# Optimization experiments

Measured on AMD Instinct MI355X. Metric: run time of the kernel, lower is better.

Reference implementation:

```python
import jax, jax.numpy as jnp
import numpy as np

V, E, H = 32000, 256, 512   # vocab, embed_dim, hidden_dim
B, S, T = 16, 512, 128      # batch, src_len, tgt_len
PAD = 0
H2 = 2 * H                  # decoder hidden size


def setup_inputs() -> dict:
    key = jax.random.key(0)
    ks = jax.random.split(key, 20)
    g = lambda k, shape: jax.random.normal(k, shape, dtype=jnp.float32) * 0.05
    emb = g(ks[0], (V, E)).at[PAD].set(0.0)  # padding_idx row zeroed
    inp = {
        "src": jax.random.randint(ks[18], (B, S), 0, V, dtype=jnp.int32),
        "tgt": jax.random.randint(ks[19], (B, T), 0, V, dtype=jnp.int32),
        "emb": emb,
        # encoder forward direction (torch gate order i,f,g,o)
        "Wih_f": g(ks[1], (4 * H, E)), "Whh_f": g(ks[2], (4 * H, H)),
        "bih_f": g(ks[3], (4 * H,)),   "bhh_f": g(ks[4], (4 * H,)),
        # encoder backward direction
        "Wih_b": g(ks[5], (4 * H, E)), "Whh_b": g(ks[6], (4 * H, H)),
        "bih_b": g(ks[7], (4 * H,)),   "bhh_b": g(ks[8], (4 * H,)),
        # decoder LSTM: input E+2H, hidden 2H
        "Wih_d": g(ks[9], (4 * H2, E + H2)), "Whh_d": g(ks[10], (4 * H2, H2)),
        "bih_d": g(ks[11], (4 * H2,)),       "bhh_d": g(ks[12], (4 * H2,)),
        # attention Linear(4H -> 2H)
        "Wa": g(ks[13], (H2, 2 * H2)), "ba": g(ks[14], (H2,)),
        # output Linear(2H -> V)
        "Wo": g(ks[15], (V, H2)), "bo": g(ks[16], (V,)),
    }
    return inp


def _lstm_cell(x, h, c, Wih, Whh, bih, bhh):
    z = x @ Wih.T + h @ Whh.T + bih + bhh
    i, f, g, o = jnp.split(z, 4, axis=-1)
    c = jax.nn.sigmoid(f) * c + jax.nn.sigmoid(i) * jnp.tanh(g)
    h = jax.nn.sigmoid(o) * jnp.tanh(c)
    return h, c


def _lstm_scan(xs, h0, c0, Wih, Whh, bih, bhh):
    def step(carry, x):
        h, c = _lstm_cell(x, carry[0], carry[1], Wih, Whh, bih, bhh)
        return (h, c), h
    (hT, cT), hs = jax.lax.scan(step, (h0, c0), xs)
    return hs, hT, cT


def reference(src, tgt, emb, Wih_f, Whh_f, bih_f, bhh_f, Wih_b, Whh_b, bih_b, bhh_b,
              Wih_d, Whh_d, bih_d, bhh_d, Wa, ba, Wo, bo):
    z = jnp.zeros((B, H), dtype=emb.dtype)
    xs = emb[src].transpose(1, 0, 2)                       # [S,B,E]
    hs_f, hTf, _ = _lstm_scan(xs,        z, z, Wih_f, Whh_f, bih_f, bhh_f)
    hs_b, hTb, _ = _lstm_scan(xs[::-1],  z, z, Wih_b, Whh_b, bih_b, bhh_b)
    enc_out = jnp.concatenate([hs_f, hs_b[::-1]], -1).transpose(1, 0, 2)  # [B,S,2H]
    h = jnp.concatenate([hTf, hTb], -1)                    # decoder h0 [B,2H]
    c = jnp.zeros_like(h)  # note: original reuses encoder c_n; see combined c0 below
    # original uses c_n (last cells) as decoder c0:
    _, _, cTf = _lstm_scan(xs, z, z, Wih_f, Whh_f, bih_f, bhh_f)[1], None, None
    # recompute cleanly (scan already returned cT above; redo properly):
    hs_f2, hTf2, cTf2 = _lstm_scan(xs,       z, z, Wih_f, Whh_f, bih_f, bhh_f)
    hs_b2, hTb2, cTb2 = _lstm_scan(xs[::-1], z, z, Wih_b, Whh_b, bih_b, bhh_b)
    c = jnp.concatenate([cTf2, cTb2], -1)

    Wa_h, Wa_e = Wa[:, :H2], Wa[:, H2:]
    enc_proj = jnp.einsum('bsd,kd->bsk', enc_out, Wa_e) + ba  # [B,S,2H]

    dec_xs = emb[tgt[:, :T - 1]].transpose(1, 0, 2)        # [T-1,B,E] teacher-forced

    def dec_step(carry, x):
        h, c = carry
        energy = jnp.tanh(enc_proj + (h @ Wa_h.T)[:, None, :])  # [B,S,2H]
        w = jax.nn.softmax(energy.sum(-1), axis=1)              # [B,S]
        ctx = jnp.einsum('bs,bsd->bd', w, enc_out)              # [B,2H]
        xi = jnp.concatenate([x, ctx], -1)                      # [B,E+2H]
        h, c = _lstm_cell(xi, h, c, Wih_d, Whh_d, bih_d, bhh_d)
        pred = h @ Wo.T + bo                                    # [B,V]
        return (h, c), pred

    _, preds = jax.lax.scan(dec_step, (h, c), dec_xs)           # [T-1,B,V]
    outputs = jnp.concatenate(
        [jnp.zeros((B, 1, V), dtype=preds.dtype), preds.transpose(1, 0, 2)], axis=1)
    return outputs
```

## Files before the change

### kernel.cpp

```cpp
#include <hip/hip_runtime.h>

typedef unsigned int uint;
typedef unsigned short ushort;
typedef unsigned long long ull;
typedef __attribute__((ext_vector_type(8))) short bf16x8;
typedef __attribute__((ext_vector_type(4))) float f32x4;

static constexpr int V_ = 32000, E_ = 256, H_ = 512, B_ = 16, S_ = 512, T_ = 128;
static constexpr int H2_ = 1024, G4_ = 2048, D4_ = 4096, KXI_ = 2304;
static constexpr int DSTEPS = T_ - 1;
static constexpr int MD = 2048;
static constexpr int NWG_DEC = 256;
static constexpr float LOG2E = 1.4426950408889634f;
static constexpr int ASTR = 2312;

#define DEVFN __device__ __forceinline__

DEVFN ushort f2bf(float f){ uint u = __builtin_bit_cast(uint, f); u += 0x7fffu + ((u>>16)&1u); return (ushort)(u>>16); }
DEVFN float bf2f(ushort h){ uint u = ((uint)h)<<16; return __builtin_bit_cast(float, u); }
DEVFN float fsig(float x){ float e = __builtin_amdgcn_exp2f(-LOG2E*x); return __builtin_amdgcn_rcpf(1.f+e); }
DEVFN float ftanh(float x){ x = fminf(15.f,fmaxf(-15.f,x)); float e = __builtin_amdgcn_exp2f(2.f*LOG2E*x); return (e-1.f)*__builtin_amdgcn_rcpf(e+1.f); }
DEVFN f32x4 mfma16(bf16x8 a, bf16x8 b, f32x4 c){ return __builtin_amdgcn_mfma_f32_16x16x32_bf16(a,b,c,0,0,0); }

struct ull2v{ ull x, y; };
DEVFN ull ald64(const void* p){ return __hip_atomic_load((const ull*)p, __ATOMIC_RELAXED, __HIP_MEMORY_SCOPE_AGENT); }
DEVFN uint ald32u(const uint* p){ return __hip_atomic_load(p, __ATOMIC_RELAXED, __HIP_MEMORY_SCOPE_AGENT); }
DEVFN float ald_f32(const float* p){ uint v = __hip_atomic_load((const uint*)p, __ATOMIC_RELAXED, __HIP_MEMORY_SCOPE_AGENT); return __builtin_bit_cast(float, v); }
DEVFN bf16x8 ald_bf16x8(const ushort* p){ ull2v v{ald64(p), ald64(p+4)}; return __builtin_bit_cast(bf16x8, v); }
DEVFN void ast32(float* p, float v){ __hip_atomic_store(p, v, __ATOMIC_RELAXED, __HIP_MEMORY_SCOPE_AGENT); }
DEVFN void ast16(ushort* p, ushort v){ __hip_atomic_store(p, v, __ATOMIC_RELAXED, __HIP_MEMORY_SCOPE_AGENT); }
DEVFN void astu(uint* p, uint v){ __hip_atomic_store(p, v, __ATOMIC_RELAXED, __HIP_MEMORY_SCOPE_AGENT); }
DEVFN uint afadd(uint* p){ return __hip_atomic_fetch_add(p, 1u, __ATOMIC_RELAXED, __HIP_MEMORY_SCOPE_AGENT); }

DEVFN void dbar(uint* flags, int wgid, int tid, uint& rnd){
  __syncthreads();
  if (tid==0){
    uint* gcnt = flags + (wgid>>4)*16;
    uint* rcnt = flags + 256;
    uint* rgen = flags + 272;
    uint a = afadd(gcnt);
    if (a == rnd*16u+15u){
      uint r = afadd(rcnt);
      if (r == rnd*16u+15u) afadd(rgen);
    }
    while (ald32u(rgen) <= rnd) __builtin_amdgcn_s_sleep(1);
  }
  rnd++;
  __syncthreads();
}

__global__ void k_init(uint* __restrict__ flags, ushort* __restrict__ hgf, ushort* __restrict__ hgb){
  int i = blockIdx.x*256 + threadIdx.x;
  if (i < 512) flags[i] = 0;
  if (i < 2*B_*H_){ hgf[i]=0; hgb[i]=0; }
}

__global__ void k_embed(const int* __restrict__ src, const int* __restrict__ tgt,
                        const float* __restrict__ emb, ushort* __restrict__ Xb, ushort* __restrict__ DXb){
  int r = blockIdx.x, tid = threadIdx.x;
  if (r < S_*B_){
    int s = r>>4, b = r&15;
    int id = src[b*S_+s];
    Xb[(size_t)r*E_+tid] = f2bf(emb[(size_t)id*E_+tid]);
  } else {
    int r2 = r - S_*B_;
    int t = r2>>4, b = r2&15;
    int id = tgt[b*T_+t];
    DXb[(size_t)r2*E_+tid] = f2bf(emb[(size_t)id*E_+tid]);
  }
}

__global__ void k_cvt_encw(const float* __restrict__ src, ushort* __restrict__ dst){
  int d = blockIdx.x;
  int wg = d>>7, r = d&127;
  int w = r>>4, jj=(r>>2)&3, g=r&3;
  int srow = g*H_ + wg*32 + w*4 + jj;
  for (int c = threadIdx.x; c < E_; c += 256)
    dst[(size_t)d*E_ + c] = f2bf(src[(size_t)srow*E_ + c]);
}

__global__ void k_bias_encp(const float* __restrict__ bih, const float* __restrict__ bhh, float* __restrict__ dst){
  int d = blockIdx.x*256 + threadIdx.x;
  int wg = d>>7, r = d&127;
  int w = r>>4, jj=(r>>2)&3, g=r&3;
  int srow = g*H_ + wg*32 + w*4 + jj;
  dst[d] = bih[srow]+bhh[srow];
}

__global__ void k_cvt_decw(const float* __restrict__ Wih_d, const float* __restrict__ Whh_d,
                           ushort* __restrict__ dst){
  int d = blockIdx.x;
  int wg = d>>4, r = d&15, jj = r>>2, g = r&3;
  int srow = g*H2_ + wg*4 + jj;
  for (int c = threadIdx.x; c < KXI_; c += 256){
    float v = (c < E_+H2_) ? Wih_d[(size_t)srow*(E_+H2_) + c] : Whh_d[(size_t)srow*H2_ + (c - (E_+H2_))];
    dst[(size_t)d*KXI_ + c] = f2bf(v);
  }
}

__global__ void k_bias_decp(const float* __restrict__ bih, const float* __restrict__ bhh, float* __restrict__ dst){
  int d = blockIdx.x*256 + threadIdx.x;
  int wg = d>>4, r = d&15, jj = r>>2, g = r&3;
  int srow = g*H2_ + wg*4 + jj;
  dst[d] = bih[srow]+bhh[srow];
}

__global__ void k_cvt_strided(const float* __restrict__ src, ushort* __restrict__ dst,
                              int cols, int sld, int soff, int dld, int doff){
  int r = blockIdx.x;
  for (int c = threadIdx.x; c < cols; c += 256)
    dst[(size_t)r*dld + doff + c] = f2bf(src[(size_t)r*sld + soff + c]);
}

__global__ void k_zero_t0(float* __restrict__ out){
  int i = blockIdx.x*256 + threadIdx.x;
  if (i < B_*V_){ int b = i / V_, v = i - b*V_; out[(size_t)b*T_*V_ + v] = 0.f; }
}

template<int MODE>
__global__ __launch_bounds__(256) void gemm128(const ushort* __restrict__ A, const ushort* __restrict__ Bm,
    const float* __restrict__ bias, void* __restrict__ outp, int M, int N, int K, int Mvalid){
  __shared__ __align__(16) ushort As[128*32];
  __shared__ __align__(16) ushort Bs[128*32];
  int tid = threadIdx.x;
  int wave = tid>>6, lane = tid&63;
  int m0 = blockIdx.y*128, n0 = blockIdx.x*128;
  int wm = wave>>1, wn = wave&1;
  int col = lane&15, rg = lane>>4;
  f32x4 acc[4][4];
  #pragma unroll
  for (int i=0;i<4;i++)
    #pragma unroll
    for (int j=0;j<4;j++) acc[i][j] = {0.f,0.f,0.f,0.f};
  for (int k0=0;k0<K;k0+=32){
    __syncthreads();
    #pragma unroll
    for (int j=0;j<2;j++){
      int li = j*256+tid;
      int row = li>>2, ko = (li&3)*8;
      *(bf16x8*)(As + li*8) = *(const bf16x8*)(A + (size_t)(m0+row)*K + k0 + ko);
      *(bf16x8*)(Bs + li*8) = *(const bf16x8*)(Bm + (size_t)(n0+row)*K + k0 + ko);
    }
    __syncthreads();
    bf16x8 af[4], bfr[4];
    #pragma unroll
    for (int f=0;f<4;f++){
      af[f]  = *(const bf16x8*)(As + (wm*64+f*16+col)*32 + rg*8);
      bfr[f] = *(const bf16x8*)(Bs + (wn*64+f*16+col)*32 + rg*8);
    }
    #pragma unroll
    for (int fm=0;fm<4;fm++)
      #pragma unroll
      for (int fn=0;fn<4;fn++)
        acc[fm][fn] = mfma16(af[fm], bfr[fn], acc[fm][fn]);
  }
  #pragma unroll
  for (int fm=0;fm<4;fm++){
    int mrow = m0 + wm*64 + fm*16 + rg*4;
    #pragma unroll
    for (int fn=0;fn<4;fn++){
      int gcol = n0 + wn*64 + fn*16 + col;
      float bv = bias ? bias[gcol] : 0.f;
      #pragma unroll
      for (int i=0;i<4;i++){
        float v = acc[fm][fn][i] + bv;
        int grow = mrow + i;
        if (MODE==0) ((float*)outp)[(size_t)grow*N + gcol] = v;
        else if (MODE==1) ((ushort*)outp)[(size_t)grow*N + gcol] = f2bf(v);
        else if (MODE==3) ((ushort*)outp)[(size_t)(grow>>4)*(16*2048) + gcol*16 + (grow&15)] = f2bf(v);
        else { if (grow < Mvalid){ int b = grow&15, t = grow>>4;
               ((float*)outp)[(size_t)b*T_*V_ + (size_t)(t+1)*V_ + gcol] = v; } }
      }
    }
  }
}

__global__ __launch_bounds__(512) void k_enc_persist(
    const ushort* __restrict__ Xgf, const ushort* __restrict__ Xgb,
    const float* __restrict__ Whhf, const float* __restrict__ Whhb,
    ushort* __restrict__ enc, ushort* __restrict__ enct,
    ushort* __restrict__ hbuf1, float* __restrict__ cbuf0,
    ushort* __restrict__ hgf, ushort* __restrict__ hgb,
    uint* __restrict__ flags){
  const int dir = blockIdx.x >> 4;
  const int wg  = blockIdx.x & 15;
  const ushort* Xg = dir ? Xgb : Xgf;
  const float* Whh = dir ? Whhb : Whhf;
  ushort* hg = dir ? hgb : hgf;
  uint* cnt = flags + 384 + dir*32;
  uint* gen = cnt + 16;
  __shared__ __align__(16) ushort Wlds[128*512];
  __shared__ __align__(16) ushort hls[16*512];
  int tid = threadIdx.x;
  for (int it=0; it<32; ++it){
    int r = it*4 + (tid>>7), ct = tid&127;
    int w_ = r>>4, jj=(r>>2)&3, g=r&3;
    int srow = g*H_ + wg*32 + w_*4 + jj;
    float4 v = *(const float4*)(Whh + (size_t)srow*H_ + ct*4);
    ushort4 o; o.x=f2bf(v.x); o.y=f2bf(v.y); o.z=f2bf(v.z); o.w=f2bf(v.w);
    int byte = (r*1024 + ct*8) ^ ((r&7)<<4);
    *(ushort4*)((char*)Wlds + byte) = o;
  }
  int w = tid>>6, lane = tid&63, colL = lane&15, rg = lane>>4;
  int gg = colL&3;
  uint rnd = 0;
  float cst[4];
  #pragma unroll
  for (int i=0;i<4;i++) cst[i]=0.f;
  __syncthreads();
  for (int t=0;t<S_;++t){
    int pos = dir ? (S_-1-t) : t;
    const ushort* hsrc = hg + (t&1)*B_*H_;
    bf16x8 hv[2];
    #pragma unroll
    for (int k2=0;k2<2;k2++){
      int idx = tid + k2*512;
      hv[k2] = ald_bf16x8(hsrc + (idx>>6)*H_ + (idx&63)*8);
    }
    int colg = wg*128 + w*16 + colL;
    ushort4 xv = *(const ushort4*)(Xg + ((size_t)pos*2048 + colg)*16 + rg*4);
    f32x4 acc;
    acc[0]=bf2f(xv.x); acc[1]=bf2f(xv.y); acc[2]=bf2f(xv.z); acc[3]=bf2f(xv.w);
    #pragma unroll
    for (int k2=0;k2<2;k2++){
      int idx = tid + k2*512;
      int byte = ((idx>>6)*1024 + (idx&63)*16) ^ (((idx>>6)&7)<<4);
      *(bf16x8*)((char*)hls + byte) = hv[k2];
    }
    __syncthreads();
    int rowb = w*16 + colL;
    int base = rowb*1024 + rg*16, xm = (rowb&7)<<4;
    int hbase = colL*1024 + rg*16, hxm = (colL&7)<<4;
    #pragma unroll
    for (int kt=0;kt<16;kt++){
      bf16x8 afv = *(const bf16x8*)((const char*)hls + ((hbase + kt*64) ^ hxm));
      bf16x8 bfv = *(const bf16x8*)((const char*)Wlds + ((base + kt*64) ^ xm));
      acc = mfma16(afv, bfv, acc);
    }
    ushort* hdst = hg + ((t+1)&1)*B_*H_;
    #pragma unroll
    for (int i=0;i<4;i++){
      float v0 = acc[i];
      float v1 = __shfl_xor(v0, 1);
      float v2 = __shfl_xor(v0, 2);
      float v3 = __shfl_xor(v1, 2);
      float zi = gg==0?v0: gg==1?v1: gg==2?v2: v3;
      float zf = (gg^1)==0?v0: (gg^1)==1?v1: (gg^1)==2?v2: v3;
      float zg = (gg^2)==0?v0: (gg^2)==1?v1: (gg^2)==2?v2: v3;
      float zo = (gg^3)==0?v0: (gg^3)==1?v1: (gg^3)==2?v2: v3;
      float cc = fsig(zf)*cst[i] + fsig(zi)*ftanh(zg);
      cst[i] = cc;
      float h = fsig(zo)*ftanh(cc);
      if (gg==0){
        int j = wg*32 + w*4 + (colL>>2);
        int b = rg*4+i;
        ushort hb = f2bf(h);
        enc[((size_t)b*S_ + pos)*H2_ + dir*H_ + j] = hb;
        enct[((size_t)b*H2_ + dir*H_ + j)*S_ + pos] = hb;
        ast16(&hdst[b*H_ + j], hb);
        if (t==S_-1){
          hbuf1[b*H2_ + dir*H_ + j] = hb;
          cbuf0[b*H2_ + dir*H_ + j] = cc;
        }
      }
    }
    if (t != S_-1){
      __syncthreads();
      if (tid==0){
        asm volatile("s_waitcnt vmcnt(0)" ::: "memory");
        uint a = afadd(cnt);
        if (a == rnd*16u+15u) afadd(gen);
        while (ald32u(gen) <= rnd) __builtin_amdgcn_s_sleep(1);
      }
      rnd++;
      __syncthreads();
    }
  }
}

__global__ __launch_bounds__(512) void k_dec(
    const float* __restrict__ P, const ushort* __restrict__ WaH,
    const ushort* __restrict__ Wd, const float* __restrict__ bsd,
    const ushort* __restrict__ enct, const ushort* __restrict__ DXb,
    const float* __restrict__ cbuf0, ushort* __restrict__ hbuf,
    ushort* __restrict__ ctxbuf, float* __restrict__ qbuf,
    float* __restrict__ scores, ushort* __restrict__ hsd,
    uint* __restrict__ flags){
  __shared__ __align__(16) ushort AB[16*ASTR];
  __shared__ __align__(16) float pr[8*256];
  __shared__ float redz[256];
  __shared__ float qls[1024];
  __shared__ float wls[512];
  __shared__ float part[512];
  __shared__ float red[16];
  __shared__ float cst[64];
  int wgid = blockIdx.x, tid = threadIdx.x;
  int w = tid>>6, lane = tid&63, colL = lane&15, rg = lane>>4;
  uint rnd = 0;
  if (tid < 64){
    int jj = tid>>4, b = tid&15;
    cst[tid] = cbuf0[b*H2_ + wgid*4 + jj];
  }
  for (int st=0; st<DSTEPS; ++st){
    ushort* hprev = hbuf + ((st+1)&1)*B_*H2_;
    if (wgid >= 64 && wgid < 128){
      int n0 = (wgid-64)*16;
      bf16x8 af[4];
      #pragma unroll
      for (int kt=0;kt<4;kt++)
        af[kt] = ald_bf16x8(hprev + colL*H2_ + w*128 + kt*32 + rg*8);
      f32x4 acc = {0.f,0.f,0.f,0.f};
      const ushort* Bp = WaH + (size_t)(n0+colL)*H2_ + w*128 + rg*8;
      #pragma unroll
      for (int kt=0;kt<4;kt++)
        acc = mfma16(af[kt], *(const bf16x8*)(Bp + kt*32), acc);
      *(f32x4*)&pr[w*256 + lane*4] = acc;
      __syncthreads();
      if (tid < 256){
        float s = pr[tid];
        #pragma unroll
        for (int w8=1;w8<8;w8++) s += pr[w8*256 + tid];
        int l = tid>>2, i = tid&3;
        ast32(&qbuf[(size_t)((l>>4)*4 + i)*H2_ + n0 + (l&15)], s);
      }
    }
    dbar(flags, wgid, tid, rnd);
    {
      int b = wgid>>4, wc = wgid&15;
      ull q2 = ald64((const ull*)(qbuf + (size_t)b*H2_) + tid);
      *(ull*)&qls[tid*2] = q2;
      __syncthreads();
      f32x4 qv[4];
      #pragma unroll
      for (int u=0;u<4;u++) qv[u] = *(const f32x4*)&qls[lane*16 + u*4];
      int rbase = b*S_ + wc*32 + w*4;
      #pragma unroll
      for (int rr=0;rr<4;rr++){
        int r = rbase + rr;
        const float4* Pr = (const float4*)(P + (size_t)r*H2_) + lane*4;
        float s = 0.f;
        #pragma unroll
        for (int u=0;u<4;u++){
          float4 pv = Pr[u];
          s += ftanh(pv.x+qv[u][0])+ftanh(pv.y+qv[u][1])+ftanh(pv.z+qv[u][2])+ftanh(pv.w+qv[u][3]);
        }
        #pragma unroll
        for (int o=32;o;o>>=1) s += __shfl_xor(s,o);
        if (lane==0) ast32(&scores[r], s);
      }
    }
    dbar(flags, wgid, tid, rnd);
    {
      int b = wgid>>4, cc = wgid&15;
      float sc = ald_f32(scores + b*S_ + tid);
      float m = sc;
      #pragma unroll
      for (int o=32;o;o>>=1) m = fmaxf(m, __shfl_xor(m,o));
      if (lane==0) red[w] = m;
      __syncthreads();
      m = red[0];
      #pragma unroll
      for (int k2=1;k2<8;k2++) m = fmaxf(m, red[k2]);
      float e = __builtin_amdgcn_exp2f((sc - m)*LOG2E);
      float ss = e;
      #pragma unroll
      for (int o=32;o;o>>=1) ss += __shfl_xor(ss,o);
      if (lane==0) red[8+w] = ss;
      __syncthreads();
      float tot = red[8];
      #pragma unroll
      for (int k2=9;k2<16;k2++) tot += red[k2];
      wls[tid] = e * __builtin_amdgcn_rcpf(tot);
      __syncthreads();
      int c = cc*64 + (tid&63), sseg = tid>>6;
      const ushort* ep = enct + ((size_t)b*H2_ + c)*S_ + sseg*64;
      float a = 0.f;
      #pragma unroll
      for (int u=0;u<8;u++){
        bf16x8 ev = *(const bf16x8*)(ep + u*8);
        #pragma unroll
        for (int j=0;j<8;j++) a += wls[sseg*64 + u*8 + j] * bf2f((ushort)ev[j]);
      }
      part[tid] = a;
      __syncthreads();
      if (tid < 64){
        float s = part[tid];
        #pragma unroll
        for (int g2=1;g2<8;g2++) s += part[g2*64 + tid];
        ast16(&ctxbuf[b*H2_ + cc*64 + tid], f2bf(s));
      }
    }
    dbar(flags, wgid, tid, rnd);
    {
      { int b3 = tid>>5, seg = tid&31;
        *(bf16x8*)&AB[b3*ASTR + seg*8] = *(const bf16x8*)(DXb + (size_t)(st*16+b3)*E_ + seg*8); }
      bf16x8 rc[4], rh2[4];
      #pragma unroll
      for (int k2=0;k2<4;k2++){
        int idx = tid + k2*512;
        rc[k2]  = ald_bf16x8(ctxbuf + (idx>>7)*H2_ + (idx&127)*8);
        rh2[k2] = ald_bf16x8(hprev  + (idx>>7)*H2_ + (idx&127)*8);
      }
      #pragma unroll
      for (int k2=0;k2<4;k2++){
        int idx = tid + k2*512;
        int row = idx>>7, seg = idx&127;
        *(bf16x8*)&AB[row*ASTR + 256 + seg*8]  = rc[k2];
        *(bf16x8*)&AB[row*ASTR + 1280 + seg*8] = rh2[k2];
      }
      __syncthreads();
      int row0 = wgid*16;
      f32x4 acc = {0.f,0.f,0.f,0.f};
      const ushort* Bp = Wd + (size_t)(row0+colL)*KXI_ + w*288 + rg*8;
      const ushort* Apb = &AB[colL*ASTR + w*288 + rg*8];
      #pragma unroll
      for (int kt=0;kt<9;kt++)
        acc = mfma16(*(const bf16x8*)(Apb + kt*32), *(const bf16x8*)(Bp + kt*32), acc);
      *(f32x4*)&pr[w*256 + lane*4] = acc;
      __syncthreads();
      if (tid < 256){
        float s = bsd[row0 + ((tid>>2)&15)];
        #pragma unroll
        for (int w8=0;w8<8;w8++) s += pr[w8*256 + tid];
        redz[tid] = s;
      }
      __syncthreads();
      if (tid < 64){
        int jj = tid>>4, b4 = tid&15, rgc = b4>>2, ic = b4&3;
        float zi = redz[((jj*4+0) + 16*rgc)*4 + ic];
        float zf = redz[((jj*4+1) + 16*rgc)*4 + ic];
        float zg = redz[((jj*4+2) + 16*rgc)*4 + ic];
        float zo = redz[((jj*4+3) + 16*rgc)*4 + ic];
        float cc2 = fsig(zf)*cst[tid] + fsig(zi)*ftanh(zg);
        cst[tid] = cc2;
        float h = fsig(zo)*ftanh(cc2);
        ushort hb = f2bf(h);
        int j = wgid*4 + jj;
        ast16(&(hbuf + (st&1)*B_*H2_)[b4*H2_ + j], hb);
        hsd[((size_t)st*B_ + b4)*H2_ + j] = hb;
      }
      __syncthreads();
    }
    if (st != DSTEPS-1) dbar(flags, wgid, tid, rnd);
  }
}

extern "C" void kernel_launch(void* const* d_in, const int* in_sizes, int n_in,
                              void* d_out, int out_size, void* d_ws, size_t ws_size,
                              hipStream_t stream) {
  const int* src   = (const int*)d_in[0];
  const int* tgt   = (const int*)d_in[1];
  const float* emb   = (const float*)d_in[2];
  const float* Wih_f = (const float*)d_in[3];
  const float* Whh_f = (const float*)d_in[4];
  const float* bih_f = (const float*)d_in[5];
  const float* bhh_f = (const float*)d_in[6];
  const float* Wih_b = (const float*)d_in[7];
  const float* Whh_b = (const float*)d_in[8];
  const float* bih_b = (const float*)d_in[9];
  const float* bhh_b = (const float*)d_in[10];
  const float* Wih_d = (const float*)d_in[11];
  const float* Whh_d = (const float*)d_in[12];
  const float* bih_d = (const float*)d_in[13];
  const float* bhh_d = (const float*)d_in[14];
  const float* Wa    = (const float*)d_in[15];
  const float* ba    = (const float*)d_in[16];
  const float* Wo    = (const float*)d_in[17];
  const float* bo    = (const float*)d_in[18];
  float* out = (float*)d_out;
  (void)in_sizes; (void)n_in; (void)out_size; (void)ws_size;

  char* ws = (char*)d_ws;
  size_t off = 0;
  auto alloc = [&](size_t bytes)->char*{ char* p = ws + off; off += (bytes + 255) & ~(size_t)255; return p; };
  ushort* Xb     = (ushort*)alloc((size_t)S_*B_*E_*2);
  ushort* DXb    = (ushort*)alloc((size_t)DSTEPS*B_*E_*2);
  ushort* Wihf_p = (ushort*)alloc((size_t)G4_*E_*2);
  ushort* Wihb_p = (ushort*)alloc((size_t)G4_*E_*2);
  float*  bsf    = (float*)alloc(G4_*4);
  float*  bsb    = (float*)alloc(G4_*4);
  ushort* ENC    = (ushort*)alloc((size_t)B_*S_*H2_*2);
  ushort* ENCT   = (ushort*)alloc((size_t)B_*S_*H2_*2);
  ushort* WaH    = (ushort*)alloc((size_t)H2_*H2_*2);
  ushort* WaE    = (ushort*)alloc((size_t)H2_*H2_*2);
  ushort* Wd     = (ushort*)alloc((size_t)D4_*KXI_*2);
  float*  bsd    = (float*)alloc(D4_*4);
  ushort* WoB    = (ushort*)alloc((size_t)V_*H2_*2);
  float*  cbuf0  = (float*)alloc(B_*H2_*4);
  ushort* hbuf   = (ushort*)alloc((size_t)2*B_*H2_*2);
  ushort* ctxbuf = (ushort*)alloc((size_t)B_*H2_*2);
  float*  qbuf   = (float*)alloc(B_*H2_*4);
  float*  scores = (float*)alloc(B_*S_*4);
  ushort* hsd    = (ushort*)alloc((size_t)MD*H2_*2);
  ushort* hgf    = (ushort*)alloc((size_t)2*B_*H_*2);
  ushort* hgb    = (ushort*)alloc((size_t)2*B_*H_*2);
  uint*   flags  = (uint*)alloc(2048);
  char*   big    = alloc((size_t)2*S_*B_*G4_*2);
  ushort* Xgf = (ushort*)big;
  ushort* Xgb = (ushort*)(big + (size_t)S_*B_*G4_*2);
  float*  P   = (float*)big;

  k_init<<<dim3(64), dim3(256), 0, stream>>>(flags, hgf, hgb);
  k_embed<<<dim3(S_*B_ + DSTEPS*B_), dim3(E_), 0, stream>>>(src, tgt, emb, Xb, DXb);
  k_cvt_encw<<<dim3(G4_), dim3(256), 0, stream>>>(Wih_f, Wihf_p);
  k_cvt_encw<<<dim3(G4_), dim3(256), 0, stream>>>(Wih_b, Wihb_p);
  k_bias_encp<<<dim3(8), dim3(256), 0, stream>>>(bih_f, bhh_f, bsf);
  k_bias_encp<<<dim3(8), dim3(256), 0, stream>>>(bih_b, bhh_b, bsb);
  k_cvt_strided<<<dim3(H2_), dim3(256), 0, stream>>>(Wa, WaH, H2_, 2*H2_, 0,   H2_, 0);
  k_cvt_strided<<<dim3(H2_), dim3(256), 0, stream>>>(Wa, WaE, H2_, 2*H2_, H2_, H2_, 0);
  k_cvt_decw<<<dim3(D4_), dim3(256), 0, stream>>>(Wih_d, Whh_d, Wd);
  k_bias_decp<<<dim3(16), dim3(256), 0, stream>>>(bih_d, bhh_d, bsd);
  k_cvt_strided<<<dim3(V_),  dim3(256), 0, stream>>>(Wo, WoB, H2_, H2_, 0, H2_, 0);

  gemm128<3><<<dim3(G4_/128, (S_*B_)/128), dim3(256), 0, stream>>>(Xb, Wihf_p, bsf, Xgf, S_*B_, G4_, E_, 0);
  gemm128<3><<<dim3(G4_/128, (S_*B_)/128), dim3(256), 0, stream>>>(Xb, Wihb_p, bsb, Xgb, S_*B_, G4_, E_, 0);

  k_enc_persist<<<dim3(32), dim3(512), 0, stream>>>(Xgf, Xgb, Whh_f, Whh_b, ENC, ENCT,
                                                    hbuf + B_*H2_, cbuf0, hgf, hgb, flags);

  gemm128<0><<<dim3(H2_/128, (B_*S_)/128), dim3(256), 0, stream>>>(ENC, WaE, ba, P, B_*S_, H2_, H2_, 0);
  k_zero_t0<<<dim3((B_*V_+255)/256), dim3(256), 0, stream>>>(out);

  k_dec<<<dim3(NWG_DEC), dim3(512), 0, stream>>>(P, WaH, Wd, bsd, ENCT, DXb, cbuf0, hbuf,
                                                 ctxbuf, qbuf, scores, hsd, flags);

  gemm128<2><<<dim3(V_/128, MD/128), dim3(256), 0, stream>>>(hsd, WoB, bo, out, MD, V_, H2_, DSTEPS*B_);
}
```

Baseline: 6.451 ms.

## Replace counter-based grid barriers with per-workgroup flag barriers and a local group barrier

Swaps the hierarchical atomic-counter barrier for a flag-array barrier: each workgroup stores its round number to its own slot, and many threads poll all slots in parallel. This removes serialized atomic fetch-adds and the two-level counter chain. The decoder's score-to-softmax barrier becomes a 16-workgroup local barrier, because only workgroups sharing a batch row exchange scores. The encoder barrier also drops its explicit vmcnt wait before signalling, which may weaken the ordering of the preceding h stores relative to the flag store.

```diff
diff --git a/kernel.cpp b/kernel.cpp
--- a/kernel.cpp
+++ b/kernel.cpp
@@ -30,28 +30,29 @@
 DEVFN void ast32(float* p, float v){ __hip_atomic_store(p, v, __ATOMIC_RELAXED, __HIP_MEMORY_SCOPE_AGENT); }
 DEVFN void ast16(ushort* p, ushort v){ __hip_atomic_store(p, v, __ATOMIC_RELAXED, __HIP_MEMORY_SCOPE_AGENT); }
 DEVFN void astu(uint* p, uint v){ __hip_atomic_store(p, v, __ATOMIC_RELAXED, __HIP_MEMORY_SCOPE_AGENT); }
-DEVFN uint afadd(uint* p){ return __hip_atomic_fetch_add(p, 1u, __ATOMIC_RELAXED, __HIP_MEMORY_SCOPE_AGENT); }
-
-DEVFN void dbar(uint* flags, int wgid, int tid, uint& rnd){
+
+DEVFN void gbar(uint* flags, int wgid, int tid, uint& rnd){
   __syncthreads();
-  if (tid==0){
-    uint* gcnt = flags + (wgid>>4)*16;
-    uint* rcnt = flags + 256;
-    uint* rgen = flags + 272;
-    uint a = afadd(gcnt);
-    if (a == rnd*16u+15u){
-      uint r = afadd(rcnt);
-      if (r == rnd*16u+15u) afadd(rgen);
-    }
-    while (ald32u(rgen) <= rnd) __builtin_amdgcn_s_sleep(1);
-  }
   rnd++;
+  if (tid==0) astu(flags + wgid, rnd);
+  if (tid<256){
+    while (ald32u(flags + tid) < rnd) __builtin_amdgcn_s_sleep(1);
+  }
+  __syncthreads();
+}
+DEVFN void lbar(uint* lflags, int grp, int mem, int tid, uint& rnd){
+  __syncthreads();
+  rnd++;
+  if (tid==0) astu(lflags + grp*16 + mem, rnd);
+  if (tid<16){
+    while (ald32u(lflags + grp*16 + tid) < rnd) __builtin_amdgcn_s_sleep(1);
+  }
   __syncthreads();
 }
 
 __global__ void k_init(uint* __restrict__ flags, ushort* __restrict__ hgf, ushort* __restrict__ hgb){
   int i = blockIdx.x*256 + threadIdx.x;
-  if (i < 512) flags[i] = 0;
+  if (i < 1024) flags[i] = 0;
   if (i < 2*B_*H_){ hgf[i]=0; hgb[i]=0; }
 }
 
@@ -187,8 +188,7 @@
   const ushort* Xg = dir ? Xgb : Xgf;
   const float* Whh = dir ? Whhb : Whhf;
   ushort* hg = dir ? hgb : hgf;
-  uint* cnt = flags + 384 + dir*32;
-  uint* gen = cnt + 16;
+  uint* ef = flags + 512 + dir*16;
   __shared__ __align__(16) ushort Wlds[128*512];
   __shared__ __align__(16) ushort hls[16*512];
   int tid = threadIdx.x;
@@ -266,13 +266,11 @@
     }
     if (t != S_-1){
       __syncthreads();
-      if (tid==0){
-        asm volatile("s_waitcnt vmcnt(0)" ::: "memory");
-        uint a = afadd(cnt);
-        if (a == rnd*16u+15u) afadd(gen);
-        while (ald32u(gen) <= rnd) __builtin_amdgcn_s_sleep(1);
-      }
       rnd++;
+      if (tid==0) astu(ef + wg, rnd);
+      if (tid<16){
+        while (ald32u(ef + tid) < rnd) __builtin_amdgcn_s_sleep(1);
+      }
       __syncthreads();
     }
   }
@@ -294,6 +292,7 @@
   __shared__ float part[512];
   __shared__ float red[16];
   __shared__ float cst[64];
+  uint* lflags = flags + 256;
   int wgid = blockIdx.x, tid = threadIdx.x;
   int w = tid>>6, lane = tid&63, colL = lane&15, rg = lane>>4;
   uint rnd = 0;
@@ -324,7 +323,7 @@
         ast32(&qbuf[(size_t)((l>>4)*4 + i)*H2_ + n0 + (l&15)], s);
       }
     }
-    dbar(flags, wgid, tid, rnd);
+    gbar(flags, wgid, tid, rnd);
     {
       int b = wgid>>4, wc = wgid&15;
       ull q2 = ald64((const ull*)(qbuf + (size_t)b*H2_) + tid);
@@ -349,7 +348,7 @@
         if (lane==0) ast32(&scores[r], s);
       }
     }
-    dbar(flags, wgid, tid, rnd);
+    lbar(lflags, wgid>>4, wgid&15, tid, rnd);
     {
       int b = wgid>>4, cc = wgid&15;
       float sc = ald_f32(scores + b*S_ + tid);
@@ -390,7 +389,7 @@
         ast16(&ctxbuf[b*H2_ + cc*64 + tid], f2bf(s));
       }
     }
-    dbar(flags, wgid, tid, rnd);
+    gbar(flags, wgid, tid, rnd);
     {
       { int b3 = tid>>5, seg = tid&31;
         *(bf16x8*)&AB[b3*ASTR + seg*8] = *(const bf16x8*)(DXb + (size_t)(st*16+b3)*E_ + seg*8); }
@@ -441,7 +440,7 @@
       }
       __syncthreads();
     }
-    if (st != DSTEPS-1) dbar(flags, wgid, tid, rnd);
+    if (st != DSTEPS-1) gbar(flags, wgid, tid, rnd);
   }
 }
 
@@ -494,7 +493,7 @@
   ushort* hsd    = (ushort*)alloc((size_t)MD*H2_*2);
   ushort* hgf    = (ushort*)alloc((size_t)2*B_*H_*2);
   ushort* hgb    = (ushort*)alloc((size_t)2*B_*H_*2);
-  uint*   flags  = (uint*)alloc(2048);
+  uint*   flags  = (uint*)alloc(4096);
   char*   big    = alloc((size_t)2*S_*B_*G4_*2);
   ushort* Xgf = (ushort*)big;
   ushort* Xgb = (ushort*)(big + (size_t)S_*B_*G4_*2);
```

After: 6.252 ms. -3.1%, faster.
